# Kernel optimization log

Hardware: AMD Instinct MI355X
Metric: run time of the kernel (lower is better)

Reference implementation:

```python
import jax, jax.numpy as jnp
import numpy as np

HEADS = 4
DIM_HEAD = 32
SCALE = 10.0
EPS = 1e-12  # F.normalize eps


def setup_inputs() -> dict:
    key = jax.random.key(0)
    k0, k1, k2 = jax.random.split(key, 3)
    b, c, h, w = 4, 256, 64, 64
    hidden = HEADS * DIM_HEAD  # 128
    x = jax.random.normal(k0, (b, c, h, w), dtype=jnp.float32)
    # 1x1 convs == per-pixel linear layers; store as [out_ch, in_ch]
    w_qkv = jax.random.normal(k1, (3 * hidden, c), dtype=jnp.float32) * (1.0 / np.sqrt(c))
    w_out = jax.random.normal(k2, (c, hidden), dtype=jnp.float32) * (1.0 / np.sqrt(hidden))
    b_out = jnp.zeros((c,), dtype=jnp.float32)
    return {"x": x, "w_qkv": w_qkv, "w_out": w_out, "b_out": b_out}


def _l2norm(t):
    # normalize along the per-head feature dim d (axis=2 of [b,h,d,n])
    n = jnp.sqrt(jnp.sum(t * t, axis=2, keepdims=True))
    return t / jnp.maximum(n, EPS)


def reference(x, w_qkv, w_out, b_out):
    b, c, h, w = x.shape
    n = h * w
    # to_qkv 1x1 conv (no bias)
    qkv = jnp.einsum('oc,bchw->bohw', w_qkv, x)          # [b, 3*hidden, h, w]
    qkv = qkv.reshape(b, 3, HEADS, DIM_HEAD, n)          # chunk dim=1 then split heads
    q, k, v = qkv[:, 0], qkv[:, 1], qkv[:, 2]            # each [b, heads, d, n]
    q = _l2norm(q)
    k = _l2norm(k)
    sim = jnp.einsum('bhdi,bhdj->bhij', q, k) * SCALE    # [b, heads, n, n]
    attn = jax.nn.softmax(sim, axis=-1)
    out = jnp.einsum('bhij,bhdj->bhid', attn, v)         # [b, heads, n, d]
    # 'b h (x y) d -> b (h d) x y'
    out = out.transpose(0, 1, 3, 2).reshape(b, HEADS * DIM_HEAD, h, w)
    # to_out 1x1 conv with bias
    return jnp.einsum('oc,bchw->bohw', w_out, out) + b_out[None, :, None, None]
```

## Files before the change

### kernel.cpp

```cpp
#include <hip/hip_runtime.h>
#include <math.h>

#define BB 4
#define CC 256
#define NHEAD 4
#define DH 32
#define NN 4096
#define HID 128

typedef _Float16 f16;
typedef _Float16 f16x8 __attribute__((ext_vector_type(8)));
typedef _Float16 f16x4 __attribute__((ext_vector_type(4)));
typedef float f32x4 __attribute__((ext_vector_type(4)));

#define QPRESCALE 14.42695041f
#define NSHIFT 14.42695041f

#if __has_builtin(__builtin_amdgcn_exp2f)
#define EXP2F(x) __builtin_amdgcn_exp2f(x)
#else
#define EXP2F(x) __expf((x)*0.6931471805599453f)
#endif

__device__ __forceinline__ f16x8 cvt8(const float* p) {
    float4 a = *(const float4*)p;
    float4 b = *(const float4*)(p + 4);
    f16x8 r;
    r[0] = (f16)a.x; r[1] = (f16)a.y; r[2] = (f16)a.z; r[3] = (f16)a.w;
    r[4] = (f16)b.x; r[5] = (f16)b.y; r[6] = (f16)b.z; r[7] = (f16)b.w;
    return r;
}

__global__ __launch_bounds__(256) void qkv_fused(const float* __restrict__ x,
                                                 const float* __restrict__ wq,
                                                 f16* __restrict__ qh,
                                                 f16* __restrict__ kh,
                                                 f16* __restrict__ vh) {
    int wave = threadIdx.x >> 6, lane = threadIdx.x & 63;
    int quad = lane >> 4, col = lane & 15;
    int b = blockIdx.z;
    int y = blockIdx.y;
    int o0 = y * 128;
    int i0 = blockIdx.x * 128 + wave * 32;
    const float* xb = x + (size_t)b * CC * NN;

    f32x4 c[8][2];
#pragma unroll
    for (int mt = 0; mt < 8; mt++)
#pragma unroll
        for (int nt = 0; nt < 2; nt++) c[mt][nt] = f32x4{0.f, 0.f, 0.f, 0.f};

#pragma unroll
    for (int k0 = 0; k0 < CC; k0 += 32) {
        f16x8 bf[2];
#pragma unroll
        for (int nt = 0; nt < 2; nt++) {
            const float* xc = xb + (size_t)(k0 + quad * 8) * NN + i0 + nt * 16 + col;
#pragma unroll
            for (int j = 0; j < 8; j++) bf[nt][j] = (f16)xc[(size_t)j * NN];
        }
#pragma unroll
        for (int mt = 0; mt < 8; mt++) {
            f16x8 a = cvt8(wq + (size_t)(o0 + mt * 16 + col) * CC + k0 + quad * 8);
            c[mt][0] = __builtin_amdgcn_mfma_f32_16x16x32_f16(a, bf[0], c[mt][0], 0, 0, 0);
            c[mt][1] = __builtin_amdgcn_mfma_f32_16x16x32_f16(a, bf[1], c[mt][1], 0, 0, 0);
        }
    }

    if (y < 2) {
        f16* dst = (y == 0) ? qh : kh;
        float pre = (y == 0) ? QPRESCALE : 1.0f;
#pragma unroll
        for (int nt = 0; nt < 2; nt++) {
#pragma unroll
            for (int hh = 0; hh < 4; hh++) {
                float ss = 0.f;
#pragma unroll
                for (int m2 = 0; m2 < 2; m2++)
#pragma unroll
                    for (int r = 0; r < 4; r++) {
                        float v = c[hh * 2 + m2][nt][r];
                        ss = fmaf(v, v, ss);
                    }
                ss += __shfl_xor(ss, 16);
                ss += __shfl_xor(ss, 32);
                float inv = pre / fmaxf(sqrtf(ss), 1e-12f);
                size_t row = ((size_t)(b * 4 + hh) * NN + i0 + nt * 16 + col) * 32;
#pragma unroll
                for (int m2 = 0; m2 < 2; m2++) {
                    f16x4 st;
#pragma unroll
                    for (int r = 0; r < 4; r++) st[r] = (f16)(c[hh * 2 + m2][nt][r] * inv);
                    *(f16x4*)(dst + row + m2 * 16 + quad * 4) = st;
                }
            }
        }
    } else {
#pragma unroll
        for (int nt = 0; nt < 2; nt++) {
            int i = i0 + nt * 16 + col;
#pragma unroll
            for (int mt = 0; mt < 8; mt++) {
                int h = mt >> 1;
                int d = (mt & 1) * 16 + quad * 4;
#pragma unroll
                for (int r = 0; r < 4; r++)
                    vh[((size_t)(b * 4 + h) * 32 + d + r) * NN + i] = (f16)c[mt][nt][r];
            }
        }
    }
}

#define KROW 40
#define VROW 72

struct KV32 {
    f16x8 k0, k1;
    f16x4 v0n0, v0n1, v1n0, v1n1;
};

__device__ __forceinline__ KV32 lds_frags(const f16* kl, const f16* vl,
                                          int jb, int col, int quad) {
    KV32 f;
    f.k0 = *(const f16x8*)(kl + (jb + col) * KROW + quad * 8);
    f.k1 = *(const f16x8*)(kl + (jb + 16 + col) * KROW + quad * 8);
    f.v0n0 = *(const f16x4*)(vl + col * VROW + jb + quad * 4);
    f.v0n1 = *(const f16x4*)(vl + (16 + col) * VROW + jb + quad * 4);
    f.v1n0 = *(const f16x4*)(vl + col * VROW + jb + 16 + quad * 4);
    f.v1n1 = *(const f16x4*)(vl + (16 + col) * VROW + jb + 16 + quad * 4);
    return f;
}

__device__ __forceinline__ f16x4 expblk(f32x4 s, float& lacc) {
    float p0 = EXP2F(s[0]), p1 = EXP2F(s[1]);
    float p2 = EXP2F(s[2]), p3 = EXP2F(s[3]);
    lacc += (p0 + p1) + (p2 + p3);
    f16x4 r;
    r[0] = (f16)p0; r[1] = (f16)p1; r[2] = (f16)p2; r[3] = (f16)p3;
    return r;
}

__device__ __forceinline__ void compute16(const KV32& f, f16x8 qB0,
                                          f32x4& o00, f32x4& o01, float& l0) {
    const f32x4 zs = {-NSHIFT, -NSHIFT, -NSHIFT, -NSHIFT};
    f32x4 s0 = __builtin_amdgcn_mfma_f32_16x16x32_f16(f.k0, qB0, zs, 0, 0, 0);
    f32x4 s1 = __builtin_amdgcn_mfma_f32_16x16x32_f16(f.k1, qB0, zs, 0, 0, 0);
    f16x4 p0 = expblk(s0, l0);
    f16x4 p1 = expblk(s1, l0);
    o00 = __builtin_amdgcn_mfma_f32_16x16x16f16(p0, f.v0n0, o00, 0, 0, 0);
    o01 = __builtin_amdgcn_mfma_f32_16x16x16f16(p0, f.v0n1, o01, 0, 0, 0);
    o00 = __builtin_amdgcn_mfma_f32_16x16x16f16(p1, f.v1n0, o00, 0, 0, 0);
    o01 = __builtin_amdgcn_mfma_f32_16x16x16f16(p1, f.v1n1, o01, 0, 0, 0);
}

__global__ __launch_bounds__(256, 4) void attn_mfma(const f16* __restrict__ qh,
                                                    const f16* __restrict__ kh,
                                                    const f16* __restrict__ vh,
                                                    f16* __restrict__ att16) {
    __shared__ __align__(16) f16 klds[2][64 * KROW];
    __shared__ __align__(16) f16 vlds[2][32 * VROW];
    int t = threadIdx.x;
    int wave = t >> 6, lane = t & 63;
    int quad = lane >> 4, col = lane & 15;

    int bid = blockIdx.x;
    int xcd = bid & 7;
    int slot = bid >> 3;
    int bh = xcd * 2 + (slot >> 6);
    int i0 = (slot & 63) * 64;
    int iw = i0 + wave * 16;

    const f16* qb = qh + (size_t)bh * NN * 32;
    const f16* kb = kh + (size_t)bh * NN * 32;
    const f16* vb = vh + (size_t)bh * 32 * NN;

    f16x8 qB0 = *(const f16x8*)(qb + (size_t)(iw + col) * 32 + quad * 8);

    f32x4 o00 = {0.f, 0.f, 0.f, 0.f}, o01 = o00;
    float l0 = 0.f;

    int ktr = t >> 2, kts = t & 3;
    int vtr = t >> 3, vts = t & 7;

    f16x8 kr, vr;
    kr = *(const f16x8*)(kb + (size_t)(0 + ktr) * 32 + kts * 8);
    vr = *(const f16x8*)(vb + (size_t)vtr * NN + 0 + vts * 8);
    *(f16x8*)(&klds[0][0] + ktr * KROW + kts * 8) = kr;
    *(f16x8*)(&vlds[0][0] + vtr * VROW + vts * 8) = vr;
    __syncthreads();
    kr = *(const f16x8*)(kb + (size_t)(64 + ktr) * 32 + kts * 8);
    vr = *(const f16x8*)(vb + (size_t)vtr * NN + 64 + vts * 8);

    for (int tile = 0; tile < 62; tile++) {
        int buf = tile & 1;
        const f16* kl = &klds[buf][0];
        const f16* vl = &vlds[buf][0];
        KV32 f0 = lds_frags(kl, vl, 0, col, quad);
        KV32 f1 = lds_frags(kl, vl, 32, col, quad);
        compute16(f0, qB0, o00, o01, l0);
        compute16(f1, qB0, o00, o01, l0);
        *(f16x8*)(&klds[buf ^ 1][0] + ktr * KROW + kts * 8) = kr;
        *(f16x8*)(&vlds[buf ^ 1][0] + vtr * VROW + vts * 8) = vr;
        __syncthreads();
        int j0 = (tile + 2) * 64;
        kr = *(const f16x8*)(kb + (size_t)(j0 + ktr) * 32 + kts * 8);
        vr = *(const f16x8*)(vb + (size_t)vtr * NN + j0 + vts * 8);
    }
    {
        KV32 f0 = lds_frags(&klds[0][0], &vlds[0][0], 0, col, quad);
        KV32 f1 = lds_frags(&klds[0][0], &vlds[0][0], 32, col, quad);
        compute16(f0, qB0, o00, o01, l0);
        compute16(f1, qB0, o00, o01, l0);
        *(f16x8*)(&klds[1][0] + ktr * KROW + kts * 8) = kr;
        *(f16x8*)(&vlds[1][0] + vtr * VROW + vts * 8) = vr;
        __syncthreads();
    }
    {
        KV32 f0 = lds_frags(&klds[1][0], &vlds[1][0], 0, col, quad);
        KV32 f1 = lds_frags(&klds[1][0], &vlds[1][0], 32, col, quad);
        compute16(f0, qB0, o00, o01, l0);
        compute16(f1, qB0, o00, o01, l0);
    }

    l0 += __shfl_xor(l0, 16); l0 += __shfl_xor(l0, 32);

    int b = bh >> 2, h = bh & 3;
    f16* ab = att16 + (size_t)b * NN * HID + h * 32;
#pragma unroll
    for (int r = 0; r < 4; r++) {
        float inv0 = __builtin_amdgcn_rcpf(__shfl(l0, quad * 4 + r));
        size_t row0 = (size_t)(iw + quad * 4 + r) * HID;
        ab[row0 + col]      = (f16)(o00[r] * inv0);
        ab[row0 + 16 + col] = (f16)(o01[r] * inv0);
    }
}

__global__ __launch_bounds__(256) void out_mfma(const f16* __restrict__ att16,
                                                const float* __restrict__ wo,
                                                const float* __restrict__ bo,
                                                float* __restrict__ out) {
    int wave = threadIdx.x >> 6, lane = threadIdx.x & 63;
    int quad = lane >> 4, col = lane & 15;
    int b = blockIdx.z;
    int i0 = (blockIdx.x * 4 + wave) * 32;
    int o0 = blockIdx.y * 128;
    const f16* ab = att16 + (size_t)b * NN * HID;

    f32x4 c[2][8];
#pragma unroll
    for (int it = 0; it < 2; it++)
#pragma unroll
        for (int ot = 0; ot < 8; ot++) c[it][ot] = f32x4{0.f, 0.f, 0.f, 0.f};

#pragma unroll
    for (int k0 = 0; k0 < HID; k0 += 32) {
        f16x8 a0 = *(const f16x8*)(ab + (size_t)(i0 + col) * HID + k0 + quad * 8);
        f16x8 a1 = *(const f16x8*)(ab + (size_t)(i0 + 16 + col) * HID + k0 + quad * 8);
#pragma unroll
        for (int ot = 0; ot < 8; ot++) {
            f16x8 bf = cvt8(wo + (size_t)(o0 + ot * 16 + col) * HID + k0 + quad * 8);
            c[0][ot] = __builtin_amdgcn_mfma_f32_16x16x32_f16(a0, bf, c[0][ot], 0, 0, 0);
            c[1][ot] = __builtin_amdgcn_mfma_f32_16x16x32_f16(a1, bf, c[1][ot], 0, 0, 0);
        }
    }

#pragma unroll
    for (int it = 0; it < 2; it++)
#pragma unroll
        for (int ot = 0; ot < 8; ot++) {
            int o = o0 + ot * 16 + col;
            float bias = bo[o];
            int i = i0 + it * 16 + quad * 4;
            float4 st = {c[it][ot][0] + bias, c[it][ot][1] + bias,
                         c[it][ot][2] + bias, c[it][ot][3] + bias};
            *(float4*)(out + ((size_t)b * CC + o) * NN + i) = st;
        }
}

extern "C" void kernel_launch(void* const* d_in, const int* in_sizes, int n_in,
                              void* d_out, int out_size, void* d_ws, size_t ws_size,
                              hipStream_t stream) {
    const float* x     = (const float*)d_in[0];
    const float* w_qkv = (const float*)d_in[1];
    const float* w_out = (const float*)d_in[2];
    const float* b_out = (const float*)d_in[3];
    float* out = (float*)d_out;

    char* ws = (char*)d_ws;
    f16* qh    = (f16*)(ws);
    f16* kh    = (f16*)(ws + (4u << 20));
    f16* vh    = (f16*)(ws + (8u << 20));
    f16* att16 = (f16*)(ws + (12u << 20));

    qkv_fused<<<dim3(NN / 128, 3, BB), 256, 0, stream>>>(x, w_qkv, qh, kh, vh);
    attn_mfma<<<dim3(1024), 256, 0, stream>>>(qh, kh, vh, att16);
    out_mfma<<<dim3(NN / 128, 2, BB), 256, 0, stream>>>(att16, w_out, b_out, out);
}
```

Before: 181.9 us.

## Split attention over keys, double query rows per wave, add combine kernel

Result: faster. 173.7 us (-4.5%).

```diff
diff --git a/kernel.cpp b/kernel.cpp
--- a/kernel.cpp
+++ b/kernel.cpp
@@ -113,6 +113,8 @@
 
 #define KROW 40
 #define VROW 72
+#define KSPLIT 2048
+#define NTILE (KSPLIT / 64)
 
 struct KV32 {
     f16x8 k0, k1;
@@ -131,32 +133,45 @@
     return f;
 }
 
-__device__ __forceinline__ f16x4 expblk(f32x4 s, float& lacc) {
-    float p0 = EXP2F(s[0]), p1 = EXP2F(s[1]);
-    float p2 = EXP2F(s[2]), p3 = EXP2F(s[3]);
-    lacc += (p0 + p1) + (p2 + p3);
+__device__ __forceinline__ f16x4 expblk(f32x4 s) {
     f16x4 r;
-    r[0] = (f16)p0; r[1] = (f16)p1; r[2] = (f16)p2; r[3] = (f16)p3;
+    r[0] = (f16)EXP2F(s[0]); r[1] = (f16)EXP2F(s[1]);
+    r[2] = (f16)EXP2F(s[2]); r[3] = (f16)EXP2F(s[3]);
     return r;
 }
 
-__device__ __forceinline__ void compute16(const KV32& f, f16x8 qB0,
-                                          f32x4& o00, f32x4& o01, float& l0) {
+__device__ __forceinline__ void compute32(const KV32& f, f16x8 qB0, f16x8 qB1,
+                                          f32x4& o00, f32x4& o01,
+                                          f32x4& o10, f32x4& o11,
+                                          f32x4& la0, f32x4& la1, f16x4 vones) {
     const f32x4 zs = {-NSHIFT, -NSHIFT, -NSHIFT, -NSHIFT};
-    f32x4 s0 = __builtin_amdgcn_mfma_f32_16x16x32_f16(f.k0, qB0, zs, 0, 0, 0);
-    f32x4 s1 = __builtin_amdgcn_mfma_f32_16x16x32_f16(f.k1, qB0, zs, 0, 0, 0);
-    f16x4 p0 = expblk(s0, l0);
-    f16x4 p1 = expblk(s1, l0);
-    o00 = __builtin_amdgcn_mfma_f32_16x16x16f16(p0, f.v0n0, o00, 0, 0, 0);
-    o01 = __builtin_amdgcn_mfma_f32_16x16x16f16(p0, f.v0n1, o01, 0, 0, 0);
-    o00 = __builtin_amdgcn_mfma_f32_16x16x16f16(p1, f.v1n0, o00, 0, 0, 0);
-    o01 = __builtin_amdgcn_mfma_f32_16x16x16f16(p1, f.v1n1, o01, 0, 0, 0);
+    f32x4 s00 = __builtin_amdgcn_mfma_f32_16x16x32_f16(f.k0, qB0, zs, 0, 0, 0);
+    f32x4 s10 = __builtin_amdgcn_mfma_f32_16x16x32_f16(f.k0, qB1, zs, 0, 0, 0);
+    f32x4 s01 = __builtin_amdgcn_mfma_f32_16x16x32_f16(f.k1, qB0, zs, 0, 0, 0);
+    f32x4 s11 = __builtin_amdgcn_mfma_f32_16x16x32_f16(f.k1, qB1, zs, 0, 0, 0);
+    f16x4 p00 = expblk(s00);
+    f16x4 p10 = expblk(s10);
+    f16x4 p01 = expblk(s01);
+    f16x4 p11 = expblk(s11);
+    o00 = __builtin_amdgcn_mfma_f32_16x16x16f16(p00, f.v0n0, o00, 0, 0, 0);
+    o01 = __builtin_amdgcn_mfma_f32_16x16x16f16(p00, f.v0n1, o01, 0, 0, 0);
+    la0 = __builtin_amdgcn_mfma_f32_16x16x16f16(p00, vones, la0, 0, 0, 0);
+    o10 = __builtin_amdgcn_mfma_f32_16x16x16f16(p10, f.v0n0, o10, 0, 0, 0);
+    o11 = __builtin_amdgcn_mfma_f32_16x16x16f16(p10, f.v0n1, o11, 0, 0, 0);
+    la1 = __builtin_amdgcn_mfma_f32_16x16x16f16(p10, vones, la1, 0, 0, 0);
+    o00 = __builtin_amdgcn_mfma_f32_16x16x16f16(p01, f.v1n0, o00, 0, 0, 0);
+    o01 = __builtin_amdgcn_mfma_f32_16x16x16f16(p01, f.v1n1, o01, 0, 0, 0);
+    la0 = __builtin_amdgcn_mfma_f32_16x16x16f16(p01, vones, la0, 0, 0, 0);
+    o10 = __builtin_amdgcn_mfma_f32_16x16x16f16(p11, f.v1n0, o10, 0, 0, 0);
+    o11 = __builtin_amdgcn_mfma_f32_16x16x16f16(p11, f.v1n1, o11, 0, 0, 0);
+    la1 = __builtin_amdgcn_mfma_f32_16x16x16f16(p11, vones, la1, 0, 0, 0);
 }
 
 __global__ __launch_bounds__(256, 4) void attn_mfma(const f16* __restrict__ qh,
                                                     const f16* __restrict__ kh,
                                                     const f16* __restrict__ vh,
-                                                    f16* __restrict__ att16) {
+                                                    float* __restrict__ opart,
+                                                    float* __restrict__ lpart) {
     __shared__ __align__(16) f16 klds[2][64 * KROW];
     __shared__ __align__(16) f16 vlds[2][32 * VROW];
     int t = threadIdx.x;
@@ -167,50 +182,55 @@
     int xcd = bid & 7;
     int slot = bid >> 3;
     int bh = xcd * 2 + (slot >> 6);
-    int i0 = (slot & 63) * 64;
-    int iw = i0 + wave * 16;
+    int rem = slot & 63;
+    int ks = rem >> 5;
+    int i0 = (rem & 31) * 128;
+    int iw = i0 + wave * 32;
+    int jbase = ks * KSPLIT;
 
     const f16* qb = qh + (size_t)bh * NN * 32;
     const f16* kb = kh + (size_t)bh * NN * 32;
     const f16* vb = vh + (size_t)bh * 32 * NN;
 
     f16x8 qB0 = *(const f16x8*)(qb + (size_t)(iw + col) * 32 + quad * 8);
-
-    f32x4 o00 = {0.f, 0.f, 0.f, 0.f}, o01 = o00;
-    float l0 = 0.f;
+    f16x8 qB1 = *(const f16x8*)(qb + (size_t)(iw + 16 + col) * 32 + quad * 8);
+
+    f32x4 o00 = {0.f, 0.f, 0.f, 0.f}, o01 = o00, o10 = o00, o11 = o00;
+    f32x4 la0 = o00, la1 = o00;
+    f16x4 vones = {(f16)1.f, (f16)1.f, (f16)1.f, (f16)1.f};
 
     int ktr = t >> 2, kts = t & 3;
     int vtr = t >> 3, vts = t & 7;
 
     f16x8 kr, vr;
-    kr = *(const f16x8*)(kb + (size_t)(0 + ktr) * 32 + kts * 8);
-    vr = *(const f16x8*)(vb + (size_t)vtr * NN + 0 + vts * 8);
+    kr = *(const f16x8*)(kb + (size_t)(jbase + ktr) * 32 + kts * 8);
+    vr = *(const f16x8*)(vb + (size_t)vtr * NN + jbase + vts * 8);
     *(f16x8*)(&klds[0][0] + ktr * KROW + kts * 8) = kr;
     *(f16x8*)(&vlds[0][0] + vtr * VROW + vts * 8) = vr;
     __syncthreads();
-    kr = *(const f16x8*)(kb + (size_t)(64 + ktr) * 32 + kts * 8);
-    vr = *(const f16x8*)(vb + (size_t)vtr * NN + 64 + vts * 8);
-
-    for (int tile = 0; tile < 62; tile++) {
+    kr = *(const f16x8*)(kb + (size_t)(jbase + 64 + ktr) * 32 + kts * 8);
+    vr = *(const f16x8*)(vb + (size_t)vtr * NN + jbase + 64 + vts * 8);
+
+    for (int tile = 0; tile < NTILE - 2; tile++) {
         int buf = tile & 1;
         const f16* kl = &klds[buf][0];
         const f16* vl = &vlds[buf][0];
         KV32 f0 = lds_frags(kl, vl, 0, col, quad);
         KV32 f1 = lds_frags(kl, vl, 32, col, quad);
-        compute16(f0, qB0, o00, o01, l0);
-        compute16(f1, qB0, o00, o01, l0);
+        compute32(f0, qB0, qB1, o00, o01, o10, o11, la0, la1, vones);
+        compute32(f1, qB0, qB1, o00, o01, o10, o11, la0, la1, vones);
         *(f16x8*)(&klds[buf ^ 1][0] + ktr * KROW + kts * 8) = kr;
         *(f16x8*)(&vlds[buf ^ 1][0] + vtr * VROW + vts * 8) = vr;
         __syncthreads();
-        int j0 = (tile + 2) * 64;
+        int j0 = jbase + (tile + 2) * 64;
         kr = *(const f16x8*)(kb + (size_t)(j0 + ktr) * 32 + kts * 8);
         vr = *(const f16x8*)(vb + (size_t)vtr * NN + j0 + vts * 8);
     }
     {
         KV32 f0 = lds_frags(&klds[0][0], &vlds[0][0], 0, col, quad);
         KV32 f1 = lds_frags(&klds[0][0], &vlds[0][0], 32, col, quad);
-        compute16(f0, qB0, o00, o01, l0);
-        compute16(f1, qB0, o00, o01, l0);
+        compute32(f0, qB0, qB1, o00, o01, o10, o11, la0, la1, vones);
+        compute32(f1, qB0, qB1, o00, o01, o10, o11, la0, la1, vones);
         *(f16x8*)(&klds[1][0] + ktr * KROW + kts * 8) = kr;
         *(f16x8*)(&vlds[1][0] + vtr * VROW + vts * 8) = vr;
         __syncthreads();
@@ -218,20 +238,47 @@
     {
         KV32 f0 = lds_frags(&klds[1][0], &vlds[1][0], 0, col, quad);
         KV32 f1 = lds_frags(&klds[1][0], &vlds[1][0], 32, col, quad);
-        compute16(f0, qB0, o00, o01, l0);
-        compute16(f1, qB0, o00, o01, l0);
-    }
-
-    l0 += __shfl_xor(l0, 16); l0 += __shfl_xor(l0, 32);
-
+        compute32(f0, qB0, qB1, o00, o01, o10, o11, la0, la1, vones);
+        compute32(f1, qB0, qB1, o00, o01, o10, o11, la0, la1, vones);
+    }
+
+    float* op = opart + (size_t)(ks * 16 + bh) * NN * 32;
+    float* lp = lpart + (size_t)(ks * 16 + bh) * NN;
+#pragma unroll
+    for (int r = 0; r < 4; r++) {
+        int q0 = iw + quad * 4 + r;
+        int q1 = iw + 16 + quad * 4 + r;
+        op[(size_t)q0 * 32 + col]      = o00[r];
+        op[(size_t)q0 * 32 + 16 + col] = o01[r];
+        op[(size_t)q1 * 32 + col]      = o10[r];
+        op[(size_t)q1 * 32 + 16 + col] = o11[r];
+        if (col == 0) { lp[q0] = la0[r]; lp[q1] = la1[r]; }
+    }
+}
+
+__global__ __launch_bounds__(256) void combine(const float* __restrict__ opart,
+                                               const float* __restrict__ lpart,
+                                               f16* __restrict__ att16) {
+    int idx = blockIdx.x * 256 + threadIdx.x;
+    int bh = idx >> 12, i = idx & 4095;
+    const float* p0 = opart + ((size_t)bh * NN + i) * 32;
+    const float* p1 = opart + ((size_t)(16 + bh) * NN + i) * 32;
+    float l = lpart[(size_t)bh * NN + i] + lpart[(size_t)(16 + bh) * NN + i];
+    float inv = 1.0f / l;
     int b = bh >> 2, h = bh & 3;
-    f16* ab = att16 + (size_t)b * NN * HID + h * 32;
-#pragma unroll
-    for (int r = 0; r < 4; r++) {
-        float inv0 = __builtin_amdgcn_rcpf(__shfl(l0, quad * 4 + r));
-        size_t row0 = (size_t)(iw + quad * 4 + r) * HID;
-        ab[row0 + col]      = (f16)(o00[r] * inv0);
-        ab[row0 + 16 + col] = (f16)(o01[r] * inv0);
+    f16* dst = att16 + ((size_t)b * NN + i) * HID + h * 32;
+#pragma unroll
+    for (int g = 0; g < 4; g++) {
+        float4 a0 = *(const float4*)(p0 + g * 8);
+        float4 a1 = *(const float4*)(p0 + g * 8 + 4);
+        float4 b0 = *(const float4*)(p1 + g * 8);
+        float4 b1 = *(const float4*)(p1 + g * 8 + 4);
+        f16x8 o8;
+        o8[0] = (f16)((a0.x + b0.x) * inv); o8[1] = (f16)((a0.y + b0.y) * inv);
+        o8[2] = (f16)((a0.z + b0.z) * inv); o8[3] = (f16)((a0.w + b0.w) * inv);
+        o8[4] = (f16)((a1.x + b1.x) * inv); o8[5] = (f16)((a1.y + b1.y) * inv);
+        o8[6] = (f16)((a1.z + b1.z) * inv); o8[7] = (f16)((a1.w + b1.w) * inv);
+        *(f16x8*)(dst + g * 8) = o8;
     }
 }
 
@@ -287,12 +334,15 @@
     float* out = (float*)d_out;
 
     char* ws = (char*)d_ws;
-    f16* qh    = (f16*)(ws);
-    f16* kh    = (f16*)(ws + (4u << 20));
-    f16* vh    = (f16*)(ws + (8u << 20));
-    f16* att16 = (f16*)(ws + (12u << 20));
+    f16* qh      = (f16*)(ws);
+    f16* kh      = (f16*)(ws + (4u << 20));
+    f16* vh      = (f16*)(ws + (8u << 20));
+    f16* att16   = (f16*)(ws + (12u << 20));
+    float* opart = (float*)(ws + (16u << 20));
+    float* lpart = (float*)(ws + (32u << 20));
 
     qkv_fused<<<dim3(NN / 128, 3, BB), 256, 0, stream>>>(x, w_qkv, qh, kh, vh);
-    attn_mfma<<<dim3(1024), 256, 0, stream>>>(qh, kh, vh, att16);
+    attn_mfma<<<dim3(1024), 256, 0, stream>>>(qh, kh, vh, opart, lpart);
+    combine<<<dim3(16 * NN / 256), 256, 0, stream>>>(opart, lpart, att16);
     out_mfma<<<dim3(NN / 128, 2, BB), 256, 0, stream>>>(att16, w_out, b_out, out);
 }
```
